# Optimization experiments

Hardware: AMD Instinct MI355X
Metric: run time of the kernel (lower is better)

## Reference

```python
import jax, jax.numpy as jnp
import numpy as np

IN_FEATURES = 4096
OUT_FEATURES = 16384
BATCH = 2
SEQ = 2048


def setup_inputs() -> dict:
    key = jax.random.key(0)
    k_x, k_s, k_sgn, k_b = jax.random.split(key, 4)
    x = jax.random.normal(k_x, (BATCH, SEQ, IN_FEATURES), dtype=jnp.float32)
    # stored: uint8-style inverse-log magnitudes in [1, 255]
    stored = jax.random.randint(k_s, (OUT_FEATURES, IN_FEATURES), 1, 256, dtype=jnp.int32)
    # sign in {0,1}; mapped to {-1,+1} inside reference
    sign = jax.random.randint(k_sgn, (OUT_FEATURES, IN_FEATURES), 0, 2, dtype=jnp.int32)
    # log range matching typical weight magnitudes exp(-8)..exp(0)
    log_min = jnp.full((1,), -8.0, dtype=jnp.float32)
    log_max = jnp.full((1,), 0.0, dtype=jnp.float32)
    bias = jax.random.normal(k_b, (OUT_FEATURES,), dtype=jnp.float32) * 0.02
    return {"x": x, "stored": stored, "sign": sign, "log_min": log_min,
            "log_max": log_max, "bias": bias}


def _dequant_qins(stored, sign, log_min, log_max):
    # reverse inverse mapping: stored in [1,255] -> normalized in [0,1]
    normalized = (255.0 - stored.astype(jnp.float32)) / 254.0
    log_weight = log_min + normalized * (log_max - log_min)
    sign_f = (2 * sign - 1).astype(jnp.float32)  # {0,1} -> {-1,+1}
    return sign_f * jnp.exp(log_weight)  # [out, in] fp32


def reference(x, stored, sign, log_min, log_max, bias):
    lmin = log_min[0]
    lmax = log_max[0]
    w = _dequant_qins(stored, sign, lmin, lmax)  # [O, I]
    # F.linear: y = x @ w.T + bias
    out = jnp.einsum('bsi,oi->bso', x, w) + bias
    return out
```

## Files before the change

### kernel.cpp

```cpp
#include <hip/hip_runtime.h>
#include <stdint.h>

#define M_DIM 4096
#define N_DIM 16384
#define K_DIM 4096
#define BM 256
#define BN 256
#define BK 64
#define NT (K_DIM / BK)

typedef __attribute__((ext_vector_type(8))) __bf16 bf16x8;
typedef __attribute__((ext_vector_type(4))) float f32x4;

__device__ __forceinline__ unsigned short f2bf(float f) {
    uint32_t u = __builtin_bit_cast(uint32_t, f);
    uint32_t r = (u + 0x7FFFu + ((u >> 16) & 1u)) >> 16;
    return (unsigned short)r;
}

union Pack8 { unsigned short h[8]; uint4 v; };

__device__ __forceinline__ void async_copy16(const void* g, void* l) {
    __builtin_amdgcn_global_load_lds((__attribute__((address_space(1))) void*)(g),
                                     (__attribute__((address_space(3))) void*)(l),
                                     16, 0, 0);
}

__global__ __launch_bounds__(256) void cast_x_kernel(const float* __restrict__ x,
                                                     unsigned short* __restrict__ xb,
                                                     int n8) {
    for (int i = blockIdx.x * blockDim.x + threadIdx.x; i < n8;
         i += gridDim.x * blockDim.x) {
        const float4* p = (const float4*)(x + (size_t)i * 8);
        float4 v0 = p[0], v1 = p[1];
        Pack8 o;
        o.h[0] = f2bf(v0.x); o.h[1] = f2bf(v0.y);
        o.h[2] = f2bf(v0.z); o.h[3] = f2bf(v0.w);
        o.h[4] = f2bf(v1.x); o.h[5] = f2bf(v1.y);
        o.h[6] = f2bf(v1.z); o.h[7] = f2bf(v1.w);
        *(uint4*)(xb + (size_t)i * 8) = o.v;
    }
}

__global__ __launch_bounds__(256) void dequant_kernel(const int* __restrict__ stored,
                                                      const int* __restrict__ sign,
                                                      const float* __restrict__ log_min,
                                                      const float* __restrict__ log_max,
                                                      unsigned short* __restrict__ wb,
                                                      int n8) {
    const float lmin = log_min[0];
    const float lrange = log_max[0] - lmin;
    for (int i = blockIdx.x * blockDim.x + threadIdx.x; i < n8;
         i += gridDim.x * blockDim.x) {
        const int4* ps = (const int4*)(stored + (size_t)i * 8);
        const int4* pg = (const int4*)(sign + (size_t)i * 8);
        int4 s0 = ps[0], s1 = ps[1];
        int4 g0 = pg[0], g1 = pg[1];
        int sv[8] = {s0.x, s0.y, s0.z, s0.w, s1.x, s1.y, s1.z, s1.w};
        int gv[8] = {g0.x, g0.y, g0.z, g0.w, g1.x, g1.y, g1.z, g1.w};
        Pack8 o;
#pragma unroll
        for (int j = 0; j < 8; ++j) {
            float nrm = (255.0f - (float)sv[j]) * (1.0f / 254.0f);
            float w = __expf(lmin + nrm * lrange);
            o.h[j] = f2bf(gv[j] ? w : -w);
        }
        *(uint4*)(wb + (size_t)i * 8) = o.v;
    }
}

__global__ __launch_bounds__(512, 1) void gemm_kernel(const unsigned short* __restrict__ A,
                                                      const unsigned short* __restrict__ W,
                                                      const float* __restrict__ bias,
                                                      float* __restrict__ C) {
    extern __shared__ char lds[];
    const int tid  = threadIdx.x;
    const int wave = tid >> 6;
    const int lane = tid & 63;
    const int l15  = lane & 15;
    const int l16  = lane >> 4;
    const int wr   = wave >> 2;
    const int wc   = wave & 3;

    const int bid = blockIdx.x;
    const int wg  = ((bid & 7) << 7) | (bid >> 3);
    const int rowBase = (wg >> 6) * BM;
    const int colBase = (wg & 63) * BN;

    f32x4 acc[8][4] = {};

    auto stage = [&](int t, int d) {
        const int kb = t * BK;
        char* base = lds + d * 65536;
#pragma unroll
        for (int u = 0; u < 4; ++u) {
            const unsigned short* g = (u < 2) ? A : W;
            const int rb = ((u < 2) ? rowBase : colBase) + (u & 1) * 128;
            char* hb = base + ((u < 2) ? 0 : 32768) + (u & 1) * 16384;
#pragma unroll
            for (int sub = 0; sub < 2; ++sub) {
                const int Ld   = (sub * 512 + tid) * 16;
                const int r    = Ld >> 7;
                const int colb = (Ld & 127) ^ ((r & 7) << 4);
                async_copy16(g + (size_t)(rb + r) * K_DIM + kb + (colb >> 1),
                             hb + (sub * 512 + wave * 64) * 16);
            }
        }
    };

    stage(0, 0);

    for (int t = 0; t < NT; ++t) {
        const int cur = t & 1;
        if (t + 1 < NT) {
            stage(t + 1, cur ^ 1);
            asm volatile("s_waitcnt vmcnt(8)" ::: "memory");
        } else {
            asm volatile("s_waitcnt vmcnt(0)" ::: "memory");
        }
        __builtin_amdgcn_s_barrier();
        asm volatile("" ::: "memory");

        const char* bA  = lds + cur * 65536 + wr * 16384;
        const char* bB  = lds + cur * 65536 + 32768 + (wc >> 1) * 16384;
        const int   brB = (wc & 1) * 64;

        bf16x8 aF[4][2];
        bf16x8 bF[2][2];
#pragma unroll
        for (int q = 0; q < 4; ++q) {
            const int mq = q >> 1, nq = q & 1;
            if (nq == 0) {
#pragma unroll
                for (int i = 0; i < 4; ++i)
#pragma unroll
                    for (int ks = 0; ks < 2; ++ks) {
                        const int r    = (mq * 4 + i) * 16 + l15;
                        const int colb = (ks * 64 + l16 * 16) ^ ((r & 7) << 4);
                        aF[i][ks] = *(const bf16x8*)(bA + (r << 7) + colb);
                    }
            }
#pragma unroll
            for (int j = 0; j < 2; ++j)
#pragma unroll
                for (int ks = 0; ks < 2; ++ks) {
                    const int r    = brB + (nq * 2 + j) * 16 + l15;
                    const int colb = (ks * 64 + l16 * 16) ^ ((r & 7) << 4);
                    bF[j][ks] = *(const bf16x8*)(bB + (r << 7) + colb);
                }
            __builtin_amdgcn_s_setprio(1);
#pragma unroll
            for (int i = 0; i < 4; ++i)
#pragma unroll
                for (int j = 0; j < 2; ++j)
#pragma unroll
                    for (int ks = 0; ks < 2; ++ks)
                        acc[mq * 4 + i][nq * 2 + j] =
                            __builtin_amdgcn_mfma_f32_16x16x32_bf16(
                                aF[i][ks], bF[j][ks], acc[mq * 4 + i][nq * 2 + j],
                                0, 0, 0);
            __builtin_amdgcn_s_setprio(0);
            asm volatile("" ::: "memory");
            __builtin_amdgcn_s_barrier();
            asm volatile("" ::: "memory");
        }
    }

#pragma unroll
    for (int m = 0; m < 8; ++m) {
        const int grow0 = rowBase + wr * 128 + m * 16 + l16 * 4;
#pragma unroll
        for (int n = 0; n < 4; ++n) {
            const int gcol = colBase + wc * 64 + n * 16 + l15;
            const float bv = bias[gcol];
#pragma unroll
            for (int r4 = 0; r4 < 4; ++r4)
                C[(size_t)(grow0 + r4) * N_DIM + gcol] = acc[m][n][r4] + bv;
        }
    }
}

extern "C" void kernel_launch(void* const* d_in, const int* in_sizes, int n_in,
                              void* d_out, int out_size, void* d_ws, size_t ws_size,
                              hipStream_t stream) {
    const float* x       = (const float*)d_in[0];
    const int*   stored  = (const int*)d_in[1];
    const int*   sign    = (const int*)d_in[2];
    const float* log_min = (const float*)d_in[3];
    const float* log_max = (const float*)d_in[4];
    const float* bias    = (const float*)d_in[5];
    float* out = (float*)d_out;

    unsigned short* Ab = (unsigned short*)d_ws;
    unsigned short* Wb = (unsigned short*)((char*)d_ws +
                          (size_t)M_DIM * K_DIM * sizeof(unsigned short));

    cast_x_kernel<<<2048, 256, 0, stream>>>(x, Ab, (M_DIM * K_DIM) / 8);
    dequant_kernel<<<4096, 256, 0, stream>>>(stored, sign, log_min, log_max, Wb,
                                             (N_DIM * K_DIM) / 8);

    hipFuncSetAttribute((const void*)gemm_kernel,
                        hipFuncAttributeMaxDynamicSharedMemorySize, 131072);
    gemm_kernel<<<dim3((M_DIM / BM) * (N_DIM / BN)), dim3(512), 131072, stream>>>(
        Ab, Wb, bias, out);
}
```

Before: 704.1 us.

## Interleave half-tile async prefetches across GEMM quadrants with two-step lookahead

Splits the per-tile global-to-LDS staging into four half-tile pieces and issues them inside the quadrant loop. A operands are prefetched two tiles ahead and B operands one tile ahead, with extra barriers and lgkmcnt waits so a buffer is only overwritten once its fragments have been read. The goal is to spread memory traffic across the compute phases and keep more loads in flight, instead of issuing one burst per tile. In exchange it adds a barrier per quadrant, and the buffer-reuse logic needs careful sync to stay correct.

```diff
diff --git a/kernel.cpp b/kernel.cpp
--- a/kernel.cpp
+++ b/kernel.cpp
@@ -25,6 +25,10 @@
                                      (__attribute__((address_space(3))) void*)(l),
                                      16, 0, 0);
 }
+
+#define BARRIER() do { asm volatile("" ::: "memory"); \
+                       __builtin_amdgcn_s_barrier();  \
+                       asm volatile("" ::: "memory"); } while (0)
 
 __global__ __launch_bounds__(256) void cast_x_kernel(const float* __restrict__ x,
                                                      unsigned short* __restrict__ xb,
@@ -89,40 +93,34 @@
 
     f32x4 acc[8][4] = {};
 
-    auto stage = [&](int t, int d) {
+    auto stage_half = [&](int t, int d, int u) {
         const int kb = t * BK;
-        char* base = lds + d * 65536;
-#pragma unroll
-        for (int u = 0; u < 4; ++u) {
-            const unsigned short* g = (u < 2) ? A : W;
-            const int rb = ((u < 2) ? rowBase : colBase) + (u & 1) * 128;
-            char* hb = base + ((u < 2) ? 0 : 32768) + (u & 1) * 16384;
-#pragma unroll
-            for (int sub = 0; sub < 2; ++sub) {
-                const int Ld   = (sub * 512 + tid) * 16;
-                const int r    = Ld >> 7;
-                const int colb = (Ld & 127) ^ ((r & 7) << 4);
-                async_copy16(g + (size_t)(rb + r) * K_DIM + kb + (colb >> 1),
-                             hb + (sub * 512 + wave * 64) * 16);
-            }
+        const unsigned short* g = (u < 2) ? A : W;
+        const int rb = ((u < 2) ? rowBase : colBase) + (u & 1) * 128;
+        char* hb = lds + d * 65536 + ((u < 2) ? 0 : 32768) + (u & 1) * 16384;
+#pragma unroll
+        for (int sub = 0; sub < 2; ++sub) {
+            const int Ld   = (sub * 512 + tid) * 16;
+            const int r    = Ld >> 7;
+            const int colb = (Ld & 127) ^ ((r & 7) << 4);
+            async_copy16(g + (size_t)(rb + r) * K_DIM + kb + (colb >> 1),
+                         hb + (sub * 512 + wave * 64) * 16);
         }
     };
 
-    stage(0, 0);
+    stage_half(0, 0, 0); stage_half(0, 0, 1);
+    stage_half(0, 0, 2); stage_half(0, 0, 3);
+    stage_half(1, 1, 0); stage_half(1, 1, 1);
 
     for (int t = 0; t < NT; ++t) {
-        const int cur = t & 1;
-        if (t + 1 < NT) {
-            stage(t + 1, cur ^ 1);
-            asm volatile("s_waitcnt vmcnt(8)" ::: "memory");
-        } else {
-            asm volatile("s_waitcnt vmcnt(0)" ::: "memory");
-        }
-        __builtin_amdgcn_s_barrier();
-        asm volatile("" ::: "memory");
-
-        const char* bA  = lds + cur * 65536 + wr * 16384;
-        const char* bB  = lds + cur * 65536 + 32768 + (wc >> 1) * 16384;
+        const int c = t & 1;
+        if (t + 1 < NT) asm volatile("s_waitcnt vmcnt(4)" ::: "memory");
+        else            asm volatile("s_waitcnt vmcnt(0)" ::: "memory");
+        BARRIER();
+        __builtin_amdgcn_sched_barrier(0);
+
+        const char* bA  = lds + c * 65536 + wr * 16384;
+        const char* bB  = lds + c * 65536 + 32768 + (wc >> 1) * 16384;
         const int   brB = (wc & 1) * 64;
 
         bf16x8 aF[4][2];
@@ -148,6 +146,15 @@
                     const int colb = (ks * 64 + l16 * 16) ^ ((r & 7) << 4);
                     bF[j][ks] = *(const bf16x8*)(bB + (r << 7) + colb);
                 }
+            if (q == 0 && t + 1 < NT) stage_half(t + 1, c ^ 1, 2);
+            if (q == 1 && t + 1 < NT) stage_half(t + 1, c ^ 1, 3);
+            if (q == 3 && t + 2 < NT) {
+                stage_half(t + 2, c, 0);
+                stage_half(t + 2, c, 1);
+            }
+            BARRIER();
+            asm volatile("s_waitcnt lgkmcnt(0)" ::: "memory");
+            __builtin_amdgcn_sched_barrier(0);
             __builtin_amdgcn_s_setprio(1);
 #pragma unroll
             for (int i = 0; i < 4; ++i)
@@ -160,9 +167,7 @@
                                 aF[i][ks], bF[j][ks], acc[mq * 4 + i][nq * 2 + j],
                                 0, 0, 0);
             __builtin_amdgcn_s_setprio(0);
-            asm volatile("" ::: "memory");
-            __builtin_amdgcn_s_barrier();
-            asm volatile("" ::: "memory");
+            BARRIER();
         }
     }
 
```

After: 654.1 us. 1.08x faster.
